# Performance work log

Hardware: AMD Instinct MI355X
Metric: run time of the kernel (lower is better)

The kernel has to match this reference:

```python
import math
import jax, jax.numpy as jnp
import numpy as np

ROUNDS = 4
BUCKET_LEN = 64
NEG_BIG = -1e9
NEG_SELF = -1e5
EPS = 1e-12


def look_back(x):
    # x: [B, n_buckets, bucket_len, ...]; prepend previous bucket (circular) along bucket_len axis
    return jnp.concatenate([jnp.roll(x, 1, axis=1), x], axis=2)


def gather_dim1(x, idx):
    # torch expand_gather: broadcast x and idx to common shape, gather along axis 1
    shape = np.broadcast_shapes(x.shape, idx.shape)
    return jnp.take_along_axis(jnp.broadcast_to(x, shape), jnp.broadcast_to(idx, shape), axis=1)


def setup_inputs() -> dict:
    key = jax.random.key(0)
    k1, k2, k3 = jax.random.split(key, 3)
    B, L, d_k = 16, 4096, 64
    n_buckets = L // BUCKET_LEN
    query = jax.random.normal(k1, (B, L, d_k), dtype=jnp.float32)
    value = jax.random.normal(k2, (B, L, d_k), dtype=jnp.float32)
    rand_matrix = jax.random.normal(k3, (B, d_k, ROUNDS, n_buckets // 2), dtype=jnp.float32)
    return {"query": query, "value": value, "rand_matrix": rand_matrix, "seed": 0}


def lsh_hashes(query, rand_matrix):
    # LocalitySensitiveHash.forward
    B, L, d_k = query.shape
    qn = query / jnp.maximum(jnp.linalg.norm(query, axis=-1, keepdims=True), EPS)
    rm = rand_matrix / jnp.linalg.norm(rand_matrix, axis=1, keepdims=True)
    mm = jnp.einsum('bld,bdrn->blrn', qn, rm)  # [B, L, rounds, n_buckets//2]
    h = jnp.argmax(jnp.concatenate([mm, -mm], axis=-1), axis=-1).astype(jnp.int32)  # [B, L, rounds]
    return h * L + jnp.arange(L, dtype=jnp.int32)[None, :, None]  # unique per position


def _lsh_attention(query, value, rand_matrix):
    B, L, d_k = query.shape
    R, bl = ROUNDS, BUCKET_LEN
    nb = L // bl

    h = lsh_hashes(query, rand_matrix)
    sorted_hashes = jnp.sort(h, axis=1)
    hash_indice = jnp.argsort(h, axis=1)               # [B, L, R]
    original_indice = jnp.argsort(hash_indice, axis=1)  # reverse_sort

    # reorder queries by hash, bucketize: [B, nb, bl, d_k, R]
    rq = gather_dim1(query[:, :, :, None], hash_indice[:, :, None, :]).reshape(B, nb, bl, d_k, R)
    lb_key = look_back(rq)
    lb_key = lb_key / jnp.maximum(jnp.linalg.norm(lb_key, axis=-2, keepdims=True), EPS)
    scores = jnp.einsum('bnidr,bnjdr->bnijr', rq, lb_key) / math.sqrt(d_k)  # [B, nb, bl, 2bl, R]

    # mask: different buckets, causal, self
    sh = sorted_hashes.reshape(B, nb, bl, R) // L  # bucket id
    scores = jnp.where(sh[..., None, :] != look_back(sh)[..., None, :, :], NEG_BIG, scores)
    qi = hash_indice.reshape(B, nb, bl, R).astype(jnp.int32)
    ki = look_back(qi)  # [B, nb, 2bl, R]
    scores = jnp.where(qi[..., None, :] < ki[..., None, :, :], NEG_BIG, scores)
    scores = jnp.where(qi[..., None, :] == ki[..., None, :, :], NEG_SELF, scores)

    # duplicate-key counting across rounds (get_dup_keys)
    ki_full = jnp.broadcast_to(ki[:, :, None, :, :], (B, nb, bl, 2 * bl, R)).reshape(B, L, 2 * bl, R)
    ki_full = gather_dim1(ki_full, original_indice[:, :, None, :])
    flat = ki_full.reshape(B, L, 2 * bl * R)
    s_idx = jnp.argsort(flat, axis=-1)
    s = jnp.take_along_axis(flat, s_idx, axis=-1)
    counts = jnp.ones_like(s)
    for i in range(1, R):
        eq = (s[..., i:] == s[..., :-i]).astype(s.dtype)
        counts = counts + jnp.pad(eq, ((0, 0), (0, 0), (i, 0))) + jnp.pad(eq, ((0, 0), (0, 0), (0, i)))
    inv = jnp.argsort(s_idx, axis=-1)
    count_key = jnp.take_along_axis(counts, inv, axis=-1).reshape(B, L, 2 * bl, R)
    count_key = gather_dim1(count_key, hash_indice[:, :, None, :])

    # duplicate-adjusted softmax
    scores = scores.reshape(B, L, 2 * bl, R)
    lse = jax.nn.logsumexp(scores, axis=2)  # [B, L, R]
    softmax_qk = jnp.exp(scores - jnp.log(count_key.astype(scores.dtype)) - lse[:, :, None, :])

    rv = gather_dim1(value[:, :, :, None], hash_indice[:, :, None, :]).reshape(B, nb, bl, d_k, R)
    sm = softmax_qk.reshape(B, nb, bl, 2 * bl, R)
    attn = jnp.einsum('bnijr,bnjdr->bnidr', sm, look_back(rv)).reshape(B, L, d_k, R)
    attn = gather_dim1(attn, original_indice[:, :, None, :])
    lse = jnp.take_along_axis(lse, original_indice, axis=1)
    round_weights = jax.nn.softmax(lse, axis=1)  # dim=1 (length) exactly as in the source
    return jnp.einsum('bldr,blr->bld', attn, round_weights)


def reference(query, value, rand_matrix, seed):
    # seed is unused by the original forward body; dropout skipped (eval mode)
    return _lsh_attention(query, value, rand_matrix)
```

## Files before the change

### kernel.cpp

```cpp
#include <hip/hip_runtime.h>
#include <math.h>

#define B_  16
#define L_  4096
#define D_  64
#define R_  4
#define NB_ 64
#define BL_ 64
#define FIXCAP 8192

typedef _Float16 f16x8 __attribute__((ext_vector_type(8)));
typedef _Float16 f16x2 __attribute__((ext_vector_type(2)));
typedef float    f32x4 __attribute__((ext_vector_type(4)));


__global__ __launch_bounds__(64) void k_rmnorm(const float* __restrict__ rm,
                                               double* __restrict__ rmn,
                                               _Float16* __restrict__ rhi_g,
                                               _Float16* __restrict__ rlo_g,
                                               int* __restrict__ fix_cnt) {
    if (blockIdx.x == 0 && threadIdx.x == 0) *fix_cnt = 0;
    int blk = blockIdx.x;
    int b = blk >> 7, r = (blk >> 5) & 3, n = blk & 31;
    int d = threadIdx.x;
    double v = (double)rm[(((size_t)b * 64 + d) * 4 + r) * 32 + n];
    double sq = v * v;
    #pragma unroll
    for (int off = 32; off > 0; off >>= 1) sq += __shfl_down(sq, off);
    double tot = __shfl(sq, 0);
    double nv = v / sqrt(tot);
    rmn[(((size_t)b * 4 + r) * 32 + n) * 64 + d] = nv;
    float f = (float)nv;
    _Float16 hi = (_Float16)f;
    size_t gi = ((size_t)b * 128 + r * 32 + n) * 64 + d;
    rhi_g[gi] = hi;
    rlo_g[gi] = (_Float16)(f - (float)hi);
}

__global__ __launch_bounds__(256, 4) void k_hash(const float* __restrict__ q,
                                                 const float* __restrict__ value,
                                                 const _Float16* __restrict__ rhi_g,
                                                 const _Float16* __restrict__ rlo_g,
                                                 int* __restrict__ h_ws,
                                                 int* __restrict__ fix_cnt,
                                                 int* __restrict__ fix_list,
                                                 _Float16* __restrict__ qhf,
                                                 _Float16* __restrict__ khf,
                                                 _Float16* __restrict__ vhf) {
    __shared__ __align__(16) char smem[36864];
    _Float16* Rhi = (_Float16*)smem;
    _Float16* Rlo = (_Float16*)(smem + 18432);
    float*    Sc  = (float*)smem;

    int blk = blockIdx.x;
    int b = blk >> 6, chunk = blk & 63;
    int tid = threadIdx.x;
    int w = tid >> 6, lane = tid & 63, quad = lane >> 4, l15 = lane & 15;

    {
        int row = chunk * 64 + (tid >> 2), sub = tid & 3;
        const float4* vp = (const float4*)(value + ((size_t)(b * L_ + row)) * 64 + sub * 16);
        f16x8 h0, h1;
        #pragma unroll
        for (int c = 0; c < 2; c++) {
            float4 t0 = vp[2 * c], t1 = vp[2 * c + 1];
            f16x8& hd = c ? h1 : h0;
            hd[0]=(_Float16)t0.x; hd[1]=(_Float16)t0.y; hd[2]=(_Float16)t0.z; hd[3]=(_Float16)t0.w;
            hd[4]=(_Float16)t1.x; hd[5]=(_Float16)t1.y; hd[6]=(_Float16)t1.z; hd[7]=(_Float16)t1.w;
        }
        _Float16* dst = vhf + ((size_t)(b * L_ + row)) * 64 + sub * 16;
        *(f16x8*)dst = h0;
        *(f16x8*)(dst + 8) = h1;
    }

    {
        int row = tid >> 1, dh = (tid & 1) * 32;
        const _Float16* sh = rhi_g + ((size_t)b * 128 + row) * 64 + dh;
        const _Float16* sl = rlo_g + ((size_t)b * 128 + row) * 64 + dh;
        #pragma unroll
        for (int g = 0; g < 4; g++) {
            *(f16x8*)&Rhi[row * 72 + dh + g * 8] = *(const f16x8*)(sh + g * 8);
            *(f16x8*)&Rlo[row * 72 + dh + g * 8] = *(const f16x8*)(sl + g * 8);
        }
    }

    int qrow = chunk * 64 + w * 16 + l15;
    const float* qp = q + ((size_t)(b * L_ + qrow)) * 64;
    float qv[16];
    #pragma unroll
    for (int kt = 0; kt < 2; kt++) {
        float4 t0 = *(const float4*)(qp + kt * 32 + quad * 8);
        float4 t1 = *(const float4*)(qp + kt * 32 + quad * 8 + 4);
        qv[8*kt+0]=t0.x; qv[8*kt+1]=t0.y; qv[8*kt+2]=t0.z; qv[8*kt+3]=t0.w;
        qv[8*kt+4]=t1.x; qv[8*kt+5]=t1.y; qv[8*kt+6]=t1.z; qv[8*kt+7]=t1.w;
    }
    f16x8 Ahi[2], Alo[2];
    #pragma unroll
    for (int kt = 0; kt < 2; kt++) {
        #pragma unroll
        for (int j = 0; j < 8; j++) {
            _Float16 hi = (_Float16)qv[8*kt+j];
            Ahi[kt][j] = hi;
            Alo[kt][j] = (_Float16)(qv[8*kt+j] - (float)hi);
        }
    }
    {
        float ss = 0.f;
        #pragma unroll
        for (int j = 0; j < 16; j++) ss += qv[j] * qv[j];
        ss += __shfl_xor(ss, 16);
        ss += __shfl_xor(ss, 32);
        float nr = sqrtf(ss); if (nr < 1e-12f) nr = 1e-12f;
        float kscale = 0.18033688f / nr;
        _Float16* qd = qhf + ((size_t)(b * L_ + qrow)) * 64;
        _Float16* kd = khf + ((size_t)(b * L_ + qrow)) * 64;
        #pragma unroll
        for (int kt = 0; kt < 2; kt++) {
            *(f16x8*)(qd + kt * 32 + quad * 8) = Ahi[kt];
            f16x8 hv;
            #pragma unroll
            for (int j = 0; j < 8; j++) hv[j] = (_Float16)(qv[8*kt+j] * kscale);
            *(f16x8*)(kd + kt * 32 + quad * 8) = hv;
        }
    }
    __syncthreads();

    f32x4 acc[8];
    #pragma unroll
    for (int jt = 0; jt < 8; jt++) acc[jt] = (f32x4){0.f, 0.f, 0.f, 0.f};
    #pragma unroll
    for (int jt = 0; jt < 8; jt++) {
        #pragma unroll
        for (int kt = 0; kt < 2; kt++) {
            f16x8 bh = *(const f16x8*)&Rhi[(jt * 16 + l15) * 72 + kt * 32 + quad * 8];
            f16x8 bl = *(const f16x8*)&Rlo[(jt * 16 + l15) * 72 + kt * 32 + quad * 8];
            acc[jt] = __builtin_amdgcn_mfma_f32_16x16x32_f16(Ahi[kt], bh, acc[jt], 0, 0, 0);
            acc[jt] = __builtin_amdgcn_mfma_f32_16x16x32_f16(Ahi[kt], bl, acc[jt], 0, 0, 0);
            acc[jt] = __builtin_amdgcn_mfma_f32_16x16x32_f16(Alo[kt], bh, acc[jt], 0, 0, 0);
        }
    }
    __syncthreads();

    #pragma unroll
    for (int jt = 0; jt < 8; jt++) {
        #pragma unroll
        for (int reg = 0; reg < 4; reg++)
            Sc[(w * 16 + quad * 4 + reg) * 133 + jt * 16 + l15] = acc[jt][reg];
    }
    __syncthreads();

    {
        int row = tid & 63, r = tid >> 6;
        const float* sp = &Sc[row * 133 + r * 32];
        float v1 = -1e30f, v2 = -1e30f; int i1 = 0;
        #pragma unroll
        for (int n = 0; n < 32; n++) {
            float v = sp[n];
            float a = fabsf(v);
            int cand = n | ((__float_as_uint(v) >> 26) & 32);
            if (a > v1) i1 = cand;
            v2 = __builtin_amdgcn_fmed3f(a, v1, v2);
            v1 = fmaxf(a, v1);
        }
        int l = chunk * 64 + row;
        h_ws[((size_t)(b * 4 + r)) * L_ + l] = i1;
        if (v1 - v2 < 4e-5f) {
            int slot = atomicAdd(fix_cnt, 1);
            if (slot < FIXCAP) fix_list[slot] = (b << 14) | (r << 12) | l;
        }
    }
}

__global__ __launch_bounds__(64) void k_fix(const float* __restrict__ q,
                                            const double* __restrict__ rmn,
                                            const int* __restrict__ fix_cnt,
                                            const int* __restrict__ fix_list,
                                            int* __restrict__ h_ws) {
    int cnt = *fix_cnt; if (cnt > FIXCAP) cnt = FIXCAP;
    int lane = threadIdx.x;
    for (int i = blockIdx.x; i < cnt; i += gridDim.x) {
        int e = fix_list[i];
        int b = e >> 14, r = (e >> 12) & 3, l = e & 4095;
        int n = lane & 31;
        const double* rp = rmn + ((size_t)(b * 4 + r)) * 2048 + n * 64;
        const float* qr = q + ((size_t)(b * L_ + l)) * 64;
        double a0 = 0.0, a1 = 0.0, a2 = 0.0, a3 = 0.0;
        #pragma unroll
        for (int d = 0; d < 64; d += 4) {
            a0 += (double)qr[d]   * rp[d];
            a1 += (double)qr[d+1] * rp[d+1];
            a2 += (double)qr[d+2] * rp[d+2];
            a3 += (double)qr[d+3] * rp[d+3];
        }
        double acc = ((a0 + a1) + (a2 + a3));
        double v = (lane < 32) ? acc : -acc;
        int idx = lane;
        #pragma unroll
        for (int off = 1; off < 64; off <<= 1) {
            double ov = __shfl_xor(v, off);
            int   oidx = __shfl_xor(idx, off);
            if (ov > v || (ov == v && oidx < idx)) { v = ov; idx = oidx; }
        }
        if (lane == 0) h_ws[((size_t)(b * 4 + r)) * L_ + l] = idx;
    }
}

__global__ __launch_bounds__(256) void k_sort(const int* __restrict__ h_ws,
                                              int* __restrict__ oi_ws) {
    __shared__ __align__(16) unsigned short cnt[64 * 257];
    __shared__ __align__(16) unsigned short oi_s[256 * 17];
    __shared__ int part[256];

    int br = blockIdx.x;
    int t = threadIdx.x;
    const int* hp = h_ws + (size_t)br * L_;

    unsigned int* cz = (unsigned int*)cnt;
    #pragma unroll
    for (int i = 0; i < 33; i++) {
        int idx = i * 256 + t;
        if (idx < 8224) cz[idx] = 0;
    }

    int key[16];
    const int4* hp4 = (const int4*)(hp + t * 16);
    #pragma unroll
    for (int g = 0; g < 4; g++) {
        int4 v = hp4[g];
        key[g*4+0] = v.x; key[g*4+1] = v.y; key[g*4+2] = v.z; key[g*4+3] = v.w;
    }
    __syncthreads();

    #pragma unroll
    for (int k = 0; k < 16; k++) {
        unsigned short* c = &cnt[key[k] * 257 + t];
        *c = (unsigned short)(*c + 1);
    }
    __syncthreads();

    int u = t & 63, s = t >> 6;
    {
        int run = 0;
        int base_idx = u * 257 + s * 64;
        #pragma unroll 16
        for (int i = 0; i < 64; i++) {
            int c = cnt[base_idx + i];
            cnt[base_idx + i] = (unsigned short)run;
            run += c;
        }
        part[s * 64 + u] = run;
    }
    __syncthreads();

    if (t < 64) {
        int p0 = part[t], p1 = part[64 + t], p2 = part[128 + t], p3 = part[192 + t];
        int tot = p0 + p1 + p2 + p3;
        int v = tot;
        #pragma unroll
        for (int off = 1; off < 64; off <<= 1) {
            int o = __shfl_up(v, off);
            if (t >= off) v += o;
        }
        int base = v - tot;
        part[t]       = base;
        part[64 + t]  = base + p0;
        part[128 + t] = base + p0 + p1;
        part[192 + t] = base + p0 + p1 + p2;
    }
    __syncthreads();

    int sbase = s * 64;
    #pragma unroll
    for (int k = 0; k < 16; k++) {
        int uk = key[k];
        unsigned short* c = &cnt[uk * 257 + t];
        int pos = part[sbase + uk] + *c;
        *c = (unsigned short)(*c + 1);
        int idx = t * 16 + k;
        oi_s[(idx >> 4) * 17 + (idx & 15)] = (unsigned short)pos;
    }
    __syncthreads();

    int* op = oi_ws + (size_t)br * L_;
    #pragma unroll
    for (int k = 0; k < 16; k++) {
        int e = k * 256 + t;
        op[e] = (int)oi_s[(e >> 4) * 17 + (e & 15)];
    }
}

__global__ __launch_bounds__(256) void k_meta(const int* __restrict__ h_ws,
                                              const int* __restrict__ oi_ws,
                                              int4* __restrict__ meta_ws) {
    int gid = blockIdx.x * 256 + threadIdx.x;
    int br = gid >> 12, p = gid & 4095;
    int b = br >> 2, rme = br & 3;
    int hh = h_ws[(size_t)br * L_ + p];
    int pack = 0, packm1 = 0, mypos = 0;
    #pragma unroll
    for (int r2 = 0; r2 < 4; r2++) {
        int o = oi_ws[((size_t)(b * 4 + r2)) * L_ + p];
        if (r2 == rme) mypos = o;
        int bk = o >> 6;
        pack   |= bk << (8 * r2);
        packm1 |= ((bk + 63) & 63) << (8 * r2);
    }
    meta_ws[(size_t)br * L_ + mypos] = make_int4(hh, p, pack, packm1);
}

__global__ __launch_bounds__(256, 4) void k_attn(const _Float16* __restrict__ qhf,
                                                 const _Float16* __restrict__ khf,
                                                 const _Float16* __restrict__ vhf,
                                                 const int4* __restrict__ meta_ws,
                                                 float* __restrict__ lse_ws,
                                                 _Float16* __restrict__ attn_ws) {
    __shared__ _Float16 Ksh[128 * 72];
    __shared__ _Float16 Vt[64 * 136];
    __shared__ int4 kmeta[128];

    int xcd = blockIdx.x & 7, slot = blockIdx.x >> 3;
    int b = xcd * 2 + (slot >> 8);
    int rem = slot & 255, n = rem >> 2, r = rem & 3;
    int tid = threadIdx.x;
    int w = tid >> 6, lane = tid & 63, quad = lane >> 4, l15 = lane & 15;
    int hibase = (b * 4 + r) * L_;
    const int4* mp = meta_ws + hibase;
    int nprev = (n + 63) & 63;

    if (tid < 128) {
        int j = tid;
        int spos = (j < 64) ? (nprev * 64 + j) : (n * 64 + (j - 64));
        kmeta[j] = mp[spos];
    }
    {
        int j = tid >> 1, dh = (tid & 1) * 32;
        int spos = (j < 64) ? (nprev * 64 + j) : (n * 64 + (j - 64));
        int ky = mp[spos].y;
        const _Float16* src = khf + ((size_t)(b * L_ + ky)) * 64 + dh;
        #pragma unroll
        for (int g = 0; g < 4; g++)
            *(f16x8*)&Ksh[j * 72 + dh + g * 8] = *(const f16x8*)(src + g * 8);
    }
    {
        int m = tid >> 2, sub = tid & 3;
        int j0 = 2 * m, j1 = 2 * m + 1;
        int sp0 = (j0 < 64) ? (nprev * 64 + j0) : (n * 64 + (j0 - 64));
        int sp1 = (j1 < 64) ? (nprev * 64 + j1) : (n * 64 + (j1 - 64));
        int y0 = mp[sp0].y, y1 = mp[sp1].y;
        const _Float16* v0 = vhf + ((size_t)(b * L_ + y0)) * 64 + sub * 16;
        const _Float16* v1 = vhf + ((size_t)(b * L_ + y1)) * 64 + sub * 16;
        f16x8 a00 = *(const f16x8*)v0, a01 = *(const f16x8*)(v0 + 8);
        f16x8 a10 = *(const f16x8*)v1, a11 = *(const f16x8*)(v1 + 8);
        #pragma unroll
        for (int d = 0; d < 8; d++) {
            f16x2 hv = { a00[d], a10[d] };
            *(f16x2*)&Vt[(sub * 16 + d) * 136 + 2 * m] = hv;
            f16x2 hw = { a01[d], a11[d] };
            *(f16x2*)&Vt[(sub * 16 + 8 + d) * 136 + 2 * m] = hw;
        }
    }

    int qy = mp[n * 64 + w * 16 + l15].y;
    const _Float16* qp = qhf + ((size_t)(b * L_ + qy)) * 64;
    f16x8 afr[2];
    afr[0] = *(const f16x8*)(qp + quad * 8);
    afr[1] = *(const f16x8*)(qp + 32 + quad * 8);
    __syncthreads();

    f32x4 acc[8];
    #pragma unroll
    for (int jt = 0; jt < 8; jt++) acc[jt] = (f32x4){0.f, 0.f, 0.f, 0.f};
    #pragma unroll
    for (int jt = 0; jt < 8; jt++) {
        #pragma unroll
        for (int kt = 0; kt < 2; kt++) {
            f16x8 bfr = *(const f16x8*)&Ksh[(jt * 16 + l15) * 72 + kt * 32 + quad * 8];
            acc[jt] = __builtin_amdgcn_mfma_f32_16x16x32_f16(afr[kt], bfr, acc[jt], 0, 0, 0);
        }
    }

    int4 qm4[4], km4[8];
    #pragma unroll
    for (int reg = 0; reg < 4; reg++) qm4[reg] = kmeta[64 + w * 16 + quad * 4 + reg];
    #pragma unroll
    for (int jt = 0; jt < 8; jt++) km4[jt] = kmeta[jt * 16 + l15];
    __syncthreads();

    _Float16* Ph = Ksh;
    float lse_r[4], inv_r[4];
    #pragma unroll
    for (int reg = 0; reg < 4; reg++) {
        float s[8];
        #pragma unroll
        for (int jt = 0; jt < 8; jt++) {
            float v = acc[jt][reg];
            if (km4[jt].x != qm4[reg].x) v = -1.4426951e9f;
            if (qm4[reg].y < km4[jt].y)  v = -1.4426951e9f;
            if (qm4[reg].y == km4[jt].y) v = -144269.50f;
            s[jt] = v;
        }
        float m = s[0];
        #pragma unroll
        for (int jt = 1; jt < 8; jt++) m = fmaxf(m, s[jt]);
        #pragma unroll
        for (int off = 1; off < 16; off <<= 1) m = fmaxf(m, __shfl_xor(m, off));
        float te[8], sum = 0.f;
        #pragma unroll
        for (int jt = 0; jt < 8; jt++) { te[jt] = __builtin_amdgcn_exp2f(s[jt] - m); sum += te[jt]; }
        #pragma unroll
        for (int off = 1; off < 16; off <<= 1) sum += __shfl_xor(sum, off);
        inv_r[reg] = __builtin_amdgcn_rcpf(sum);
        lse_r[reg] = m * 0.6931472f + __logf(sum);
        int i = w * 16 + quad * 4 + reg;
        #pragma unroll
        for (int jt = 0; jt < 8; jt++) {
            int z1 = km4[jt].z ^ qm4[reg].z;
            int z2 = km4[jt].z ^ qm4[reg].w;
            int nz = __popc((z1 + 0x7f7f7f7f) & 0x80808080)
                   + __popc((z2 + 0x7f7f7f7f) & 0x80808080);
            float p = te[jt] * __builtin_amdgcn_rcpf((float)(8 - nz));
            Ph[i * 136 + jt * 16 + l15] = (_Float16)p;
        }
    }
    if (l15 == 0) {
        #pragma unroll
        for (int reg = 0; reg < 4; reg++)
            lse_ws[hibase + qm4[reg].y] = lse_r[reg];
    }
    __syncthreads();

    f32x4 oacc[4];
    #pragma unroll
    for (int nt = 0; nt < 4; nt++) oacc[nt] = (f32x4){0.f, 0.f, 0.f, 0.f};
    #pragma unroll
    for (int kt = 0; kt < 4; kt++) {
        f16x8 pa = *(const f16x8*)&Ph[(w * 16 + l15) * 136 + kt * 32 + quad * 8];
        #pragma unroll
        for (int nt = 0; nt < 4; nt++) {
            f16x8 vb = *(const f16x8*)&Vt[(nt * 16 + l15) * 136 + kt * 32 + quad * 8];
            oacc[nt] = __builtin_amdgcn_mfma_f32_16x16x32_f16(pa, vb, oacc[nt], 0, 0, 0);
        }
    }
    #pragma unroll
    for (int reg = 0; reg < 4; reg++) {
        size_t base = (((size_t)(b * 4 + r)) * L_ + qm4[reg].y) * 64;
        #pragma unroll
        for (int nt = 0; nt < 4; nt++)
            attn_ws[base + nt * 16 + l15] = (_Float16)(oacc[nt][reg] * inv_r[reg]);
    }
}

__global__ __launch_bounds__(256) void k_rw(const float* __restrict__ lse_ws,
                                            float* __restrict__ rwmax,
                                            float* __restrict__ rwsum) {
    __shared__ float  red[256];
    __shared__ double redd[256];
    int br = blockIdx.x;
    const float* lp = lse_ws + (size_t)br * L_;
    int t = threadIdx.x;
    float m = -1e30f;
    for (int k = t; k < L_; k += 256) m = fmaxf(m, lp[k]);
    red[t] = m; __syncthreads();
    for (int s2 = 128; s2 > 0; s2 >>= 1) {
        if (t < s2) red[t] = fmaxf(red[t], red[t + s2]);
        __syncthreads();
    }
    float mm = red[0];
    double s = 0.0;
    for (int k = t; k < L_; k += 256) s += (double)expf(lp[k] - mm);
    redd[t] = s; __syncthreads();
    for (int s2 = 128; s2 > 0; s2 >>= 1) {
        if (t < s2) redd[t] += redd[t + s2];
        __syncthreads();
    }
    if (t == 0) { rwmax[br] = mm; rwsum[br] = (float)redd[0]; }
}

__global__ __launch_bounds__(256) void k_out(const _Float16* __restrict__ attn_ws,
                                             const float* __restrict__ lse_ws,
                                             const float* __restrict__ rwmax,
                                             const float* __restrict__ rwsum,
                                             float* __restrict__ out) {
    int gid = blockIdx.x * 256 + threadIdx.x;
    int g = gid & 7;
    size_t row = (size_t)(gid >> 3);
    int b = (int)(row >> 12), l = (int)(row & 4095);
    float o[8];
    #pragma unroll
    for (int k = 0; k < 8; k++) o[k] = 0.f;
    #pragma unroll
    for (int r = 0; r < 4; r++) {
        int br = b * 4 + r;
        float wgt = __expf(lse_ws[(size_t)br * L_ + l] - rwmax[br])
                  * __builtin_amdgcn_rcpf(rwsum[br]);
        f16x8 av = *(const f16x8*)&attn_ws[(((size_t)br * L_ + l) << 6) + g * 8];
        #pragma unroll
        for (int k = 0; k < 8; k++) o[k] += (float)av[k] * wgt;
    }
    float4* op = (float4*)(out + row * 64 + g * 8);
    op[0] = make_float4(o[0], o[1], o[2], o[3]);
    op[1] = make_float4(o[4], o[5], o[6], o[7]);
}

extern "C" void kernel_launch(void* const* d_in, const int* in_sizes, int n_in,
                              void* d_out, int out_size, void* d_ws, size_t ws_size,
                              hipStream_t stream) {
    const float* query = (const float*)d_in[0];
    const float* value = (const float*)d_in[1];
    const float* rm    = (const float*)d_in[2];
    char* ws = (char*)d_ws;
    double*    rmn    = (double*)ws;
    int*       h_ws   = (int*)(ws + ((size_t)1 << 20));
    int*       oi_ws  = (int*)(ws + ((size_t)3 << 20));
    float*     lse_ws = (float*)(ws + ((size_t)4 << 20));
    float*     rwmax  = (float*)(ws + ((size_t)5 << 20));
    float*     rwsum  = (float*)(ws + ((size_t)5 << 20) + 256);
    int*       fix_cnt= (int*)(ws + ((size_t)5 << 20) + 512);
    int*       fix_list=(int*)(ws + ((size_t)5 << 20) + 1024);
    _Float16*  attn_ws= (_Float16*)(ws + ((size_t)6 << 20));
    _Float16*  rhi_g  = (_Float16*)(ws + ((size_t)40 << 20));
    _Float16*  rlo_g  = (_Float16*)(ws + ((size_t)40 << 20) + ((size_t)1 << 19));
    int4*      meta_ws= (int4*)(ws + ((size_t)41 << 20));
    _Float16*  qhf    = (_Float16*)(ws + ((size_t)45 << 20));
    _Float16*  khf    = (_Float16*)(ws + ((size_t)53 << 20));
    _Float16*  vhf    = (_Float16*)(ws + ((size_t)61 << 20));
    float*     out    = (float*)d_out;

    hipLaunchKernelGGL(k_rmnorm, dim3(2048), dim3(64),  0, stream, rm, rmn, rhi_g, rlo_g, fix_cnt);
    hipLaunchKernelGGL(k_hash,   dim3(1024), dim3(256), 0, stream, query, value, rhi_g, rlo_g,
                       h_ws, fix_cnt, fix_list, qhf, khf, vhf);
    hipLaunchKernelGGL(k_fix,    dim3(64),   dim3(64),  0, stream, query, rmn,
                       fix_cnt, fix_list, h_ws);
    hipLaunchKernelGGL(k_sort,   dim3(64),   dim3(256), 0, stream, h_ws, oi_ws);
    hipLaunchKernelGGL(k_meta,   dim3(1024), dim3(256), 0, stream, h_ws, oi_ws, meta_ws);
    hipLaunchKernelGGL(k_attn,   dim3(4096), dim3(256), 0, stream,
                       qhf, khf, vhf, meta_ws, lse_ws, attn_ws);
    hipLaunchKernelGGL(k_rw,     dim3(64),   dim3(256), 0, stream, lse_ws, rwmax, rwsum);
    hipLaunchKernelGGL(k_out,    dim3(2048), dim3(256), 0, stream,
                       attn_ws, lse_ws, rwmax, rwsum, out);
}
```

Baseline: 164.6 us.

## Emit sorted-order index in sort, coalesce meta writes, stage attention output through LDS

The sort kernel now also writes the inverse permutation (hash_indice), so the meta kernel can write its entries sequentially instead of scattering them. The attention kernel loads each meta entry once into shared memory and reuses it for the V and Q gathers rather than re-reading global memory. The output tile is staged through LDS so that each row goes out as 16-byte vector stores instead of scalar half stores. It also raises wave priority around the MFMA loops; the cost is an extra barrier, more shared memory in the sort kernel, and a new 1 MB workspace buffer.

```diff
diff --git a/kernel.cpp b/kernel.cpp
--- a/kernel.cpp
+++ b/kernel.cpp
@@ -206,9 +206,11 @@
 }
 
 __global__ __launch_bounds__(256) void k_sort(const int* __restrict__ h_ws,
+                                              int* __restrict__ hi_ws,
                                               int* __restrict__ oi_ws) {
     __shared__ __align__(16) unsigned short cnt[64 * 257];
     __shared__ __align__(16) unsigned short oi_s[256 * 17];
+    __shared__ __align__(16) unsigned short hi_s[4096];
     __shared__ int part[256];
 
     int br = blockIdx.x;
@@ -278,34 +280,37 @@
         *c = (unsigned short)(*c + 1);
         int idx = t * 16 + k;
         oi_s[(idx >> 4) * 17 + (idx & 15)] = (unsigned short)pos;
-    }
-    __syncthreads();
-
-    int* op = oi_ws + (size_t)br * L_;
+        hi_s[pos] = (unsigned short)idx;
+    }
+    __syncthreads();
+
+    int* op  = oi_ws + (size_t)br * L_;
+    int* hp2 = hi_ws + (size_t)br * L_;
     #pragma unroll
     for (int k = 0; k < 16; k++) {
         int e = k * 256 + t;
-        op[e] = (int)oi_s[(e >> 4) * 17 + (e & 15)];
+        op[e]  = (int)oi_s[(e >> 4) * 17 + (e & 15)];
+        hp2[e] = (int)hi_s[e];
     }
 }
 
 __global__ __launch_bounds__(256) void k_meta(const int* __restrict__ h_ws,
+                                              const int* __restrict__ hi_ws,
                                               const int* __restrict__ oi_ws,
                                               int4* __restrict__ meta_ws) {
     int gid = blockIdx.x * 256 + threadIdx.x;
-    int br = gid >> 12, p = gid & 4095;
-    int b = br >> 2, rme = br & 3;
+    int br = gid >> 12, spos = gid & 4095;
+    int b = br >> 2;
+    int p = hi_ws[(size_t)br * L_ + spos];
     int hh = h_ws[(size_t)br * L_ + p];
-    int pack = 0, packm1 = 0, mypos = 0;
+    int pack = 0, packm1 = 0;
     #pragma unroll
     for (int r2 = 0; r2 < 4; r2++) {
-        int o = oi_ws[((size_t)(b * 4 + r2)) * L_ + p];
-        if (r2 == rme) mypos = o;
-        int bk = o >> 6;
+        int bk = oi_ws[((size_t)(b * 4 + r2)) * L_ + p] >> 6;
         pack   |= bk << (8 * r2);
         packm1 |= ((bk + 63) & 63) << (8 * r2);
     }
-    meta_ws[(size_t)br * L_ + mypos] = make_int4(hh, p, pack, packm1);
+    meta_ws[(size_t)br * L_ + spos] = make_int4(hh, p, pack, packm1);
 }
 
 __global__ __launch_bounds__(256, 4) void k_attn(const _Float16* __restrict__ qhf,
@@ -327,26 +332,21 @@
     const int4* mp = meta_ws + hibase;
     int nprev = (n + 63) & 63;
 
-    if (tid < 128) {
-        int j = tid;
-        int spos = (j < 64) ? (nprev * 64 + j) : (n * 64 + (j - 64));
-        kmeta[j] = mp[spos];
-    }
     {
         int j = tid >> 1, dh = (tid & 1) * 32;
         int spos = (j < 64) ? (nprev * 64 + j) : (n * 64 + (j - 64));
-        int ky = mp[spos].y;
-        const _Float16* src = khf + ((size_t)(b * L_ + ky)) * 64 + dh;
+        int4 me = mp[spos];
+        if (dh == 0) kmeta[j] = me;
+        const _Float16* src = khf + ((size_t)(b * L_ + me.y)) * 64 + dh;
         #pragma unroll
         for (int g = 0; g < 4; g++)
             *(f16x8*)&Ksh[j * 72 + dh + g * 8] = *(const f16x8*)(src + g * 8);
     }
+    __syncthreads();
+
     {
         int m = tid >> 2, sub = tid & 3;
-        int j0 = 2 * m, j1 = 2 * m + 1;
-        int sp0 = (j0 < 64) ? (nprev * 64 + j0) : (n * 64 + (j0 - 64));
-        int sp1 = (j1 < 64) ? (nprev * 64 + j1) : (n * 64 + (j1 - 64));
-        int y0 = mp[sp0].y, y1 = mp[sp1].y;
+        int y0 = kmeta[2 * m].y, y1 = kmeta[2 * m + 1].y;
         const _Float16* v0 = vhf + ((size_t)(b * L_ + y0)) * 64 + sub * 16;
         const _Float16* v1 = vhf + ((size_t)(b * L_ + y1)) * 64 + sub * 16;
         f16x8 a00 = *(const f16x8*)v0, a01 = *(const f16x8*)(v0 + 8);
@@ -360,16 +360,16 @@
         }
     }
 
-    int qy = mp[n * 64 + w * 16 + l15].y;
+    int qy = kmeta[64 + w * 16 + l15].y;
     const _Float16* qp = qhf + ((size_t)(b * L_ + qy)) * 64;
     f16x8 afr[2];
     afr[0] = *(const f16x8*)(qp + quad * 8);
     afr[1] = *(const f16x8*)(qp + 32 + quad * 8);
-    __syncthreads();
 
     f32x4 acc[8];
     #pragma unroll
     for (int jt = 0; jt < 8; jt++) acc[jt] = (f32x4){0.f, 0.f, 0.f, 0.f};
+    __builtin_amdgcn_s_setprio(1);
     #pragma unroll
     for (int jt = 0; jt < 8; jt++) {
         #pragma unroll
@@ -378,6 +378,7 @@
             acc[jt] = __builtin_amdgcn_mfma_f32_16x16x32_f16(afr[kt], bfr, acc[jt], 0, 0, 0);
         }
     }
+    __builtin_amdgcn_s_setprio(0);
 
     int4 qm4[4], km4[8];
     #pragma unroll
@@ -432,6 +433,7 @@
     f32x4 oacc[4];
     #pragma unroll
     for (int nt = 0; nt < 4; nt++) oacc[nt] = (f32x4){0.f, 0.f, 0.f, 0.f};
+    __builtin_amdgcn_s_setprio(1);
     #pragma unroll
     for (int kt = 0; kt < 4; kt++) {
         f16x8 pa = *(const f16x8*)&Ph[(w * 16 + l15) * 136 + kt * 32 + quad * 8];
@@ -441,12 +443,28 @@
             oacc[nt] = __builtin_amdgcn_mfma_f32_16x16x32_f16(pa, vb, oacc[nt], 0, 0, 0);
         }
     }
-    #pragma unroll
-    for (int reg = 0; reg < 4; reg++) {
-        size_t base = (((size_t)(b * 4 + r)) * L_ + qm4[reg].y) * 64;
-        #pragma unroll
-        for (int nt = 0; nt < 4; nt++)
-            attn_ws[base + nt * 16 + l15] = (_Float16)(oacc[nt][reg] * inv_r[reg]);
+    __builtin_amdgcn_s_setprio(0);
+    __syncthreads();
+
+    _Float16* Pout = Ksh;
+    #pragma unroll
+    for (int nt = 0; nt < 4; nt++) {
+        #pragma unroll
+        for (int reg = 0; reg < 4; reg++) {
+            int i = w * 16 + quad * 4 + reg;
+            Pout[i * 72 + nt * 16 + l15] = (_Float16)(oacc[nt][reg] * inv_r[reg]);
+        }
+    }
+    __syncthreads();
+
+    {
+        int row = tid >> 2, part = tid & 3;
+        int y = kmeta[64 + row].y;
+        _Float16* dst = attn_ws + ((size_t)hibase + y) * 64;
+        f16x8 v0 = *(const f16x8*)&Pout[row * 72 + part * 8];
+        f16x8 v1 = *(const f16x8*)&Pout[row * 72 + 32 + part * 8];
+        *(f16x8*)(dst + part * 8) = v0;
+        *(f16x8*)(dst + 32 + part * 8) = v1;
     }
 }
 
@@ -511,6 +529,7 @@
     char* ws = (char*)d_ws;
     double*    rmn    = (double*)ws;
     int*       h_ws   = (int*)(ws + ((size_t)1 << 20));
+    int*       hi_ws  = (int*)(ws + ((size_t)2 << 20));
     int*       oi_ws  = (int*)(ws + ((size_t)3 << 20));
     float*     lse_ws = (float*)(ws + ((size_t)4 << 20));
     float*     rwmax  = (float*)(ws + ((size_t)5 << 20));
@@ -531,8 +550,8 @@
                        h_ws, fix_cnt, fix_list, qhf, khf, vhf);
     hipLaunchKernelGGL(k_fix,    dim3(64),   dim3(64),  0, stream, query, rmn,
                        fix_cnt, fix_list, h_ws);
-    hipLaunchKernelGGL(k_sort,   dim3(64),   dim3(256), 0, stream, h_ws, oi_ws);
-    hipLaunchKernelGGL(k_meta,   dim3(1024), dim3(256), 0, stream, h_ws, oi_ws, meta_ws);
+    hipLaunchKernelGGL(k_sort,   dim3(64),   dim3(256), 0, stream, h_ws, hi_ws, oi_ws);
+    hipLaunchKernelGGL(k_meta,   dim3(1024), dim3(256), 0, stream, h_ws, hi_ws, oi_ws, meta_ws);
     hipLaunchKernelGGL(k_attn,   dim3(4096), dim3(256), 0, stream,
                        qhf, khf, vhf, meta_ws, lse_ws, attn_ws);
     hipLaunchKernelGGL(k_rw,     dim3(64),   dim3(256), 0, stream, lse_ws, rwmax, rwsum);
```

Result: no change. 162.9 us (-1.0%).
